# Kernel tuning notes

Hardware: AMD Instinct MI355X
Metric: run time of the kernel (lower is better)

The kernel has to match this reference:

```python
import jax, jax.numpy as jnp
import numpy as np


def _scan_dir(x, Wk, Wr, b):
    # x: (B,H,W,C) already flipped for the direction; Wk:(C,4U) Wr:(U,4U) b:(4U,)
    B, H, W, C = x.shape
    U = Wr.shape[0]
    Dmax = min(H, W)          # max anti-diagonal length
    D = H + W - 1             # number of anti-diagonals
    dt = x.dtype
    k = jnp.arange(Dmax)

    def step(carry, d):
        h1, c1, h2, c2 = carry            # diag d-1 and d-2 buffers, (B,Dmax,U)
        i0 = jnp.maximum(0, d - (W - 1))  # first row on diag d
        i1 = jnp.minimum(H - 1, d)        # last row on diag d
        rows = i0 + k
        cols = d - rows
        mask = rows <= i1                 # valid lanes on this diagonal
        rs = jnp.clip(rows, 0, H - 1)
        cs = jnp.clip(cols, 0, W - 1)
        x_diag = x[:, rs, cs, :]          # (B,Dmax,C)
        i0p = jnp.maximum(0, d - W)       # i0 of diag d-1
        i0pp = jnp.maximum(0, d - 1 - W)  # i0 of diag d-2

        def nb(buf, r_nb, lane0, extra):
            v = mask & extra
            lane = jnp.clip(r_nb - lane0, 0, Dmax - 1)
            g = jnp.take(buf, lane, axis=1)
            return jnp.where(v[None, :, None], g, jnp.zeros_like(g)), v

        up_ok = rows - 1 >= 0
        left_ok = cols - 1 >= 0
        h_up, v_up = nb(h1, rows - 1, i0p, up_ok)        # (i-1, j)   on diag d-1
        h_left, v_left = nb(h1, rows, i0p, left_ok)      # (i, j-1)   on diag d-1
        h_ul, v_ul = nb(h2, rows - 1, i0pp, up_ok & left_ok)  # (i-1,j-1) diag d-2
        c_up, _ = nb(c1, rows - 1, i0p, up_ok)
        c_left, _ = nb(c1, rows, i0p, left_ok)
        c_ul, _ = nb(c2, rows - 1, i0pp, up_ok & left_ok)

        cnt = (v_up.astype(dt) + v_left.astype(dt) + v_ul.astype(dt))[None, :, None]
        cnt = jnp.maximum(cnt, jnp.asarray(1.0, dt))
        h_prev = (h_up + h_left + h_ul) / cnt
        c_prev = (c_up + c_left + c_ul) / cnt

        # keras LSTMCell math, gate order i,f,g,o
        z = x_diag @ Wk + h_prev @ Wr + b
        zi, zf, zg, zo = jnp.split(z, 4, axis=-1)
        c_new = jax.nn.sigmoid(zf) * c_prev + jax.nn.sigmoid(zi) * jnp.tanh(zg)
        h_new = jax.nn.sigmoid(zo) * jnp.tanh(c_new)
        m = mask[None, :, None]
        h_new = jnp.where(m, h_new, jnp.zeros_like(h_new))
        c_new = jnp.where(m, c_new, jnp.zeros_like(c_new))
        return (h_new, c_new, h1, c1), h_new

    z0 = jnp.zeros((B, Dmax, U), dt)
    _, hs = jax.lax.scan(step, (z0, z0, z0, z0), jnp.arange(D))  # (D,B,Dmax,U)

    # scatter diagonal buffers back into the (B,H,W,U) grid (static indices)
    d_arr = np.arange(D)[:, None]
    kk = np.arange(Dmax)[None, :]
    rows_all = np.maximum(0, d_arr - (W - 1)) + kk
    cols_all = d_arr - rows_all
    valid = rows_all <= np.minimum(H - 1, d_arr)
    rws = np.where(valid, rows_all, H)   # invalid lanes -> padding row H
    cws = np.where(valid, cols_all, 0)
    out = jnp.zeros((B, H + 1, W, U), dt)
    out = out.at[:, rws, cws].set(jnp.transpose(hs, (1, 0, 2, 3)))
    return out[:, :H]


_FLIPS = [(False, False), (False, True), (True, False), (True, True)]  # SE,SW,NE,NW


def _forward(x, Wk, Wr, b):
    outs = []
    for i, (fh, fw) in enumerate(_FLIPS):
        xx = x
        if fh:
            xx = xx[:, ::-1]
        if fw:
            xx = xx[:, :, ::-1]
        o = _scan_dir(xx, Wk[i], Wr[i], b[i])
        if fw:
            o = o[:, :, ::-1]
        if fh:
            o = o[:, ::-1]
        outs.append(o)
    return jnp.concatenate(outs, axis=-1)


def setup_inputs() -> dict:
    key = jax.random.key(0)
    k0, k1, k2, k3 = jax.random.split(key, 4)
    B, H, W, C, U = 4, 128, 128, 64, 64
    x = jax.random.normal(k0, (B, H, W, C), jnp.float32)
    Wk = jax.random.normal(k1, (4, C, 4 * U), jnp.float32) * 0.08
    Wr = jax.random.normal(k2, (4, U, 4 * U), jnp.float32) * 0.08
    b = jax.random.normal(k3, (4, 4 * U), jnp.float32) * 0.02
    return {"x": x, "Wk": Wk, "Wr": Wr, "b": b}


def reference(x, Wk, Wr, b):
    return _forward(x, Wk, Wr, b)
```

## Files before the change

### kernel.cpp

```cpp
#include <hip/hip_runtime.h>

typedef __bf16 bf16x8 __attribute__((ext_vector_type(8)));
typedef __bf16 bf16x4 __attribute__((ext_vector_type(4)));
typedef float f32x4 __attribute__((ext_vector_type(4)));
typedef unsigned long long u64;

#define NCH 8
#define CELLS 16
#define NG 256
#define L2E 1.44269504089f
#define RDEPTH 16
#define NLINK (16 * 7)
#define RING_U64 (NLINK * RDEPTH * 64)
#define PROG_OFF (RING_U64 * 8)

__device__ __forceinline__ unsigned short f2bfbits(float f) {
  __bf16 b = (__bf16)f;
  return __builtin_bit_cast(unsigned short, b);
}
__device__ __forceinline__ float bfbits2f(unsigned short s) {
  return (float)__builtin_bit_cast(__bf16, s);
}
__device__ __forceinline__ void barrier_lds() {
  asm volatile("s_waitcnt lgkmcnt(0)" ::: "memory");
  __builtin_amdgcn_s_barrier();
}
__device__ __forceinline__ int hix(int row, int byteoff) {
  return row * 128 + (byteoff ^ ((row & 7) << 4));
}

__global__ __launch_bounds__(512, 1) void mdrnn_kernel(
    const float* __restrict__ x, const float* __restrict__ Wk,
    const float* __restrict__ Wr, const float* __restrict__ bias,
    float* __restrict__ out, char* __restrict__ ws) {
  __shared__ __align__(16) unsigned char xt[3][CELLS * 128];
  __shared__ __align__(16) unsigned char Pbuf[2][CELLS * 128];
  __shared__ __align__(16) unsigned char gbh[8 * 128];
  __shared__ __align__(16) float gbc[8 * 64];
  __shared__ __align__(16) float zbuf[2][4096];
  __shared__ __align__(16) u64 pubbuf[2][64];

  u64* __restrict__ ring = (u64*)ws;
  int* __restrict__ prog = (int*)(ws + PROG_OFF);

  const int tid = threadIdx.x;
  const bool isComp = (tid < 256);
  const int L = tid & 63;
  const int lo16 = L & 15;
  const int hi16 = L >> 4;
  const int wq = (tid >> 6) & 3;
  const int u = wq * 16 + lo16;
  const int hm0 = (tid >> 4) & 15;
  const int hq16 = tid & 15;

  const int ch = blockIdx.x >> 4;
  const int g = blockIdx.x & 15;
  const int f = g >> 2;
  const int bb = g & 3;
  const int fh = (f >> 1) & 1;
  const int fw = f & 1;
  const int R0 = ch * CELLS;
  const int D1 = R0 + 142;
  const int linkDn = g * 7 + ch - 1;
  const int linkUp = g * 7 + ch;

  for (int i = tid; i < 3 * CELLS * 32; i += 512) ((int*)xt)[i] = 0;
  for (int i = tid; i < 2 * CELLS * 32; i += 512) ((int*)Pbuf)[i] = 0;
  for (int i = tid; i < 8 * 32; i += 512) ((int*)gbh)[i] = 0;
  for (int i = tid; i < 8 * 64; i += 512) gbc[i] = 0.f;

  float bsc[4] = {0.f, 0.f, 0.f, 0.f};
  bf16x8 wkh[4][2], wrh[4][2], wrl[4][2];
  int oidx[4];
  int oStep = 0, cbase = 0;
  int o_ph0 = 0, o_ph1 = 0;
  int o_pw[4] = {0, 0, 0, 0};
  if (isComp) {
    const float* Wrf = Wr + f * (64 * NG);
#pragma unroll
    for (int t = 0; t < 4; ++t) {
      const float st = (t == 2) ? (2.f * L2E) : L2E;
#pragma unroll
      for (int kt = 0; kt < 2; ++kt)
#pragma unroll
        for (int jj = 0; jj < 8; ++jj) {
          int k = kt * 32 + hi16 * 8 + jj;
          float vr = Wrf[k * NG + t * 64 + u] * st;
          __bf16 vh = (__bf16)vr;
          wrh[t][kt][jj] = vh;
          wrl[t][kt][jj] = (__bf16)(vr - (float)vh);
        }
    }
    const int ccStep = fw ? -1 : 1;
#pragma unroll
    for (int j = 0; j < 4; ++j) {
      int ro = R0 + hi16 * 4 + j;
      int rr = fh ? 127 - ro : ro;
      int c0 = R0 - ro;
      oidx[j] = ((bb * 128 + rr) * 128 + (fw ? 127 - c0 : c0)) * NG + f * 64 + u;
      o_pw[j] = hix(hi16 * 4 + j, u * 2);
    }
    oStep = ccStep * NG;
    cbase = -hi16 * 4;
    o_ph0 = hix(lo16, hi16 * 16);
    o_ph1 = hix(lo16, 64 + hi16 * 16);
  } else {
    const float* Wkf = Wk + f * (64 * NG);
#pragma unroll
    for (int t = 0; t < 4; ++t) {
      const float st = (t == 2) ? (2.f * L2E) : L2E;
      bsc[t] = bias[f * NG + t * 64 + u] * st;
#pragma unroll
      for (int kt = 0; kt < 2; ++kt)
#pragma unroll
        for (int jj = 0; jj < 8; ++jj) {
          int k = kt * 32 + hi16 * 8 + jj;
          wkh[t][kt][jj] = (__bf16)(Wkf[k * NG + t * 64 + u] * st);
        }
    }
  }
  const int o_ax0 = hix(lo16, hi16 * 16);
  const int o_ax1 = hix(lo16, 64 + hi16 * 16);

  const int ccStepH = fw ? -1 : 1;
  const int rx = R0 + hm0;
  const int rrx = fh ? 127 - rx : rx;
  int cx = R0 - rx;
  int xidx = ((bb * 128 + rrx) * 128 + (fw ? 127 - cx : cx)) * 64 + hq16 * 4;
  const int xStep = ccStepH * 64;
  float4 px;
  bool pxv = false;
  auto ldg = [&]() {
    pxv = ((unsigned)cx <= 127u);
    px = make_float4(0.f, 0.f, 0.f, 0.f);
    if (pxv) px = *(const float4*)(x + xidx);
    xidx += xStep;
    ++cx;
  };
  auto stx = [&](unsigned char* buf) {
    if (pxv) {
      bf16x4 pk;
      pk[0] = (__bf16)px.x; pk[1] = (__bf16)px.y;
      pk[2] = (__bf16)px.z; pk[3] = (__bf16)px.w;
      *(bf16x4*)(buf + hix(hm0, hq16 * 8)) = pk;
    }
  };
  auto accx = [&](const unsigned char* xp, int bi) {
    bf16x8 a0 = *(const bf16x8*)(xp + o_ax0);
    bf16x8 a1 = *(const bf16x8*)(xp + o_ax1);
    float* zw = &zbuf[bi][0] + (wq * 64 + L) * 4;
#pragma unroll
    for (int t = 0; t < 4; ++t) {
      f32x4 az = (f32x4){bsc[t], bsc[t], bsc[t], bsc[t]};
      az = __builtin_amdgcn_mfma_f32_16x16x32_bf16(a0, wkh[t][0], az, 0, 0, 0);
      az = __builtin_amdgcn_mfma_f32_16x16x32_bf16(a1, wkh[t][1], az, 0, 0, 0);
      *(f32x4*)(zw + t * 1024) = az;
    }
  };

  __syncthreads();

  if (!isComp) {
    ldg();
    stx(&xt[R0 % 3][0]);
    ldg();
  }
  __syncthreads();

  if (!isComp) {
    stx(&xt[(R0 + 1) % 3][0]);
    ldg();
    accx(&xt[R0 % 3][0], R0 & 1);
    if (wq == 0 && ch > 0) {
#pragma unroll
      for (int k = 0; k < 4; ++k) {
        const int q = R0 - 1 + k;
        u64* src = ring + ((linkDn * RDEPTH + (q & (RDEPTH - 1))) << 6) + L;
        u64 v;
        int spin = 0;
        for (;;) {
          v = __hip_atomic_load(src, __ATOMIC_RELAXED, __HIP_MEMORY_SCOPE_AGENT);
          if ((unsigned short)(v >> 48) == (unsigned short)q ||
              spin >= (1 << 22))
            break;
          ++spin;
          __builtin_amdgcn_s_sleep(2);
        }
        *(unsigned short*)(gbh + (q & 7) * 128 + L * 2) =
            (unsigned short)(v >> 32);
        gbc[(q & 7) * 64 + L] = __uint_as_float((unsigned)v);
        if (k == 0)
          *(unsigned short*)(&Pbuf[(R0 + 1) & 1][0] + L * 2) =
              (unsigned short)(v >> 32);
      }
      if (L == 0)
        __hip_atomic_store(&prog[linkDn * 16], R0 + 2, __ATOMIC_RELAXED,
                           __HIP_MEMORY_SCOPE_AGENT);
    }
  }
  __syncthreads();

  f32x4 zacc[4];
  float hnprev[4];
  float csj[4];
  float puv[4];
  int gateSeen = 0;
  if (isComp) {
    const float* zb = &zbuf[R0 & 1][0] + (wq * 64 + L) * 4;
#pragma unroll
    for (int t = 0; t < 4; ++t) zacc[t] = *(const f32x4*)(zb + t * 1024);
    const float cu0 = gbc[((R0 - 1) & 7) * 64 + u];
#pragma unroll
    for (int j = 0; j < 4; ++j) {
      const float ci = (hi16 == 0 && j == 0) ? cu0 : 0.f;
      csj[j] = ci;
      puv[j] = ci;
      hnprev[j] = 0.f;
    }
    __builtin_amdgcn_s_setprio(1);
  } else {
    accx(&xt[(R0 + 1) % 3][0], (R0 + 1) & 1);
    stx(&xt[(R0 + 2) % 3][0]);
    ldg();
  }
  __syncthreads();

  unsigned char* Pc = &Pbuf[R0 & 1][0];
  unsigned char* Pp = &Pbuf[(R0 + 1) & 1][0];
  unsigned char* xA = &xt[(R0 + 2) % 3][0];
  unsigned char* xB = &xt[R0 % 3][0];
  unsigned char* xC = &xt[(R0 + 1) % 3][0];

  for (int d = R0; d <= D1; ++d) {
    if (isComp) {
      bf16x8 pa0 = *(const bf16x8*)(Pp + o_ph0);
      bf16x8 pa1 = *(const bf16x8*)(Pp + o_ph1);
      const float gh1 = bfbits2f(*(const unsigned short*)(gbh + (d & 7) * 128 + u * 2));
      const float gh2 = bfbits2f(*(const unsigned short*)(gbh + ((d - 1) & 7) * 128 + u * 2));
      const float gc1 = gbc[(d & 7) * 64 + u];
#pragma unroll
      for (int t = 0; t < 4; ++t)
        zacc[t] = __builtin_amdgcn_mfma_f32_16x16x32_bf16(pa0, wrh[t][0], zacc[t], 0, 0, 0);
#pragma unroll
      for (int t = 0; t < 4; ++t)
        zacc[t] = __builtin_amdgcn_mfma_f32_16x16x32_bf16(pa1, wrh[t][1], zacc[t], 0, 0, 0);
#pragma unroll
      for (int t = 0; t < 4; ++t)
        zacc[t] = __builtin_amdgcn_mfma_f32_16x16x32_bf16(pa0, wrl[t][0], zacc[t], 0, 0, 0);
#pragma unroll
      for (int t = 0; t < 4; ++t)
        zacc[t] = __builtin_amdgcn_mfma_f32_16x16x32_bf16(pa1, wrl[t][1], zacc[t], 0, 0, 0);

      const bool pubW = (ch < NCH - 1) && (d >= R0 + 15);

      float hcur[4], cnew[4];
      {
        const int lm = hi16 * 4 + 3;
        const int cj = cbase - 3;
        const bool ok = ((unsigned)cj <= 127u);
        const float inv = (cj == 0 || (R0 + lm) == 0) ? 1.f : (1.f / 3.f);
        const float cpj = csj[3] * inv;
        const float e1 = __builtin_amdgcn_exp2f(-zacc[1][3]);
        const float e2 = __builtin_amdgcn_exp2f(-zacc[0][3]);
        const float e3 = __builtin_amdgcn_exp2f(zacc[2][3]);
        float cn = cpj * __builtin_amdgcn_rcpf(1.f + e1) +
                   (e3 - 1.f) * __builtin_amdgcn_rcpf((1.f + e2) * (1.f + e3));
        const float e4 = __builtin_amdgcn_exp2f(-zacc[3][3]);
        const float e5 = __builtin_amdgcn_exp2f(2.f * L2E * cn);
        float hn = (e5 - 1.f) * __builtin_amdgcn_rcpf((1.f + e4) * (1.f + e5));
        if (pubW && lm == CELLS - 1)
          pubbuf[d & 1][u] = ((u64)(unsigned short)d << 48) |
                             ((u64)f2bfbits(hn) << 32) |
                             (u64)__float_as_uint(cn);
        hn = ok ? hn : 0.f;
        cn = ok ? cn : 0.f;
        hcur[3] = hn;
        cnew[3] = cn;
        if (ok) out[oidx[3]] = hn;
      }
      const unsigned pk =
          ((unsigned)f2bfbits(hcur[3]) << 16) | f2bfbits(hnprev[3]);
      const unsigned pku = __shfl((int)pk, (L - 16) & 63);
      const float up_c = __shfl(cnew[3], (L - 16) & 63);
#pragma unroll
      for (int jj = 0; jj < 3; ++jj) {
        const int j = 2 - jj;
        const int lm = hi16 * 4 + j;
        const int cj = cbase - j;
        const bool ok = ((unsigned)cj <= 127u);
        const float inv = (cj == 0 || (R0 + lm) == 0) ? 1.f : (1.f / 3.f);
        const float cpj = csj[j] * inv;
        const float e1 = __builtin_amdgcn_exp2f(-zacc[1][j]);
        const float e2 = __builtin_amdgcn_exp2f(-zacc[0][j]);
        const float e3 = __builtin_amdgcn_exp2f(zacc[2][j]);
        float cn = cpj * __builtin_amdgcn_rcpf(1.f + e1) +
                   (e3 - 1.f) * __builtin_amdgcn_rcpf((1.f + e2) * (1.f + e3));
        const float e4 = __builtin_amdgcn_exp2f(-zacc[3][j]);
        const float e5 = __builtin_amdgcn_exp2f(2.f * L2E * cn);
        float hn = (e5 - 1.f) * __builtin_amdgcn_rcpf((1.f + e4) * (1.f + e5));
        hn = ok ? hn : 0.f;
        cn = ok ? cn : 0.f;
        hcur[j] = hn;
        cnew[j] = cn;
        if (ok) out[oidx[j]] = hn;
      }
      const float up_h = bfbits2f((unsigned short)(pku >> 16));
      const float up_hp = bfbits2f((unsigned short)(pku & 0xffff));

#pragma unroll
      for (int j = 0; j < 4; ++j) {
        const float hup = j ? hcur[j - 1] : (hi16 ? up_h : gh1);
        const float hulp = j ? hnprev[j - 1] : (hi16 ? up_hp : gh2);
        const float sPj =
            ((cbase + 1 == j) || (R0 == 0 && hi16 == 0 && j == 0))
                ? 1.f : (1.f / 3.f);
        *(unsigned short*)(Pc + o_pw[j]) =
            f2bfbits(sPj * (hup + hcur[j] + hulp));
        const float cun = j ? cnew[j - 1] : (hi16 ? up_c : gc1);
        csj[j] = cun + cnew[j] + puv[j];
        puv[j] = cun;
      }
#pragma unroll
      for (int j = 0; j < 4; ++j) {
        hnprev[j] = hcur[j];
        oidx[j] += oStep;
      }
      ++cbase;

      const float* zb = &zbuf[(d + 1) & 1][0] + (wq * 64 + L) * 4;
#pragma unroll
      for (int t = 0; t < 4; ++t) zacc[t] = *(const f32x4*)(zb + t * 1024);
    } else {
      const bool meAct = (ch > 0) && (wq == ((d - R0) & 1));
      const int q = d + 3;
      const bool qLive = meAct && (q <= R0 + 126);
      const u64* qs = ring + ((linkDn * RDEPTH + (q & (RDEPTH - 1))) << 6) + L;
      u64 qv = 0;
      if (qLive)
        qv = __hip_atomic_load(qs, __ATOMIC_RELAXED, __HIP_MEMORY_SCOPE_AGENT);

      if (wq == 0 && ch < NCH - 1) {
        const int pd = d - 1;
        if (pd >= R0 + 15) {
          if (pd >= R0 + 15 + RDEPTH && gateSeen < pd - RDEPTH) {
            int spin = 0;
            do {
              gateSeen = __hip_atomic_load(&prog[linkUp * 16], __ATOMIC_RELAXED,
                                           __HIP_MEMORY_SCOPE_AGENT);
              if (gateSeen < pd - RDEPTH) __builtin_amdgcn_s_sleep(1);
            } while (gateSeen < pd - RDEPTH && ++spin < (1 << 22));
          }
          u64 v = pubbuf[(d - 1) & 1][L];
          u64* dst = ring + ((linkUp * RDEPTH + (pd & (RDEPTH - 1))) << 6) + L;
          __hip_atomic_store(dst, v, __ATOMIC_RELAXED,
                             __HIP_MEMORY_SCOPE_AGENT);
        }
      }
      accx(xA, (d + 2) & 1);
      stx(xB);
      ldg();
      if (qLive) {
        int spin = 0;
        while ((unsigned short)(qv >> 48) != (unsigned short)q &&
               spin < (1 << 22)) {
          ++spin;
          __builtin_amdgcn_s_sleep(1);
          qv = __hip_atomic_load(qs, __ATOMIC_RELAXED,
                                 __HIP_MEMORY_SCOPE_AGENT);
        }
        *(unsigned short*)(gbh + (q & 7) * 128 + L * 2) =
            (unsigned short)(qv >> 32);
        gbc[(q & 7) * 64 + L] = __uint_as_float((unsigned)qv);
      }
      if (meAct && L == 0)
        __hip_atomic_store(&prog[linkDn * 16], min(d + 3, R0 + 126),
                           __ATOMIC_RELAXED, __HIP_MEMORY_SCOPE_AGENT);
    }

    {
      unsigned char* t0 = xA; xA = xB; xB = xC; xC = t0;
      unsigned char* t1 = Pc; Pc = Pp; Pp = t1;
    }
    barrier_lds();
  }

  if (!isComp && wq == 0 && ch < NCH - 1) {
    const int pd = D1;
    if (pd >= R0 + 15 + RDEPTH && gateSeen < pd - RDEPTH) {
      int spin = 0;
      do {
        gateSeen = __hip_atomic_load(&prog[linkUp * 16], __ATOMIC_RELAXED,
                                     __HIP_MEMORY_SCOPE_AGENT);
        if (gateSeen < pd - RDEPTH) __builtin_amdgcn_s_sleep(1);
      } while (gateSeen < pd - RDEPTH && ++spin < (1 << 22));
    }
    u64 v = pubbuf[D1 & 1][L];
    u64* dst = ring + ((linkUp * RDEPTH + (pd & (RDEPTH - 1))) << 6) + L;
    __hip_atomic_store(dst, v, __ATOMIC_RELAXED, __HIP_MEMORY_SCOPE_AGENT);
  }
}

extern "C" void kernel_launch(void* const* d_in, const int* in_sizes, int n_in,
                              void* d_out, int out_size, void* d_ws, size_t ws_size,
                              hipStream_t stream) {
  const float* x = (const float*)d_in[0];
  const float* Wk = (const float*)d_in[1];
  const float* Wr = (const float*)d_in[2];
  const float* b = (const float*)d_in[3];
  float* out = (float*)d_out;
  hipMemsetAsync(d_ws, 0, PROG_OFF + NLINK * 16 * sizeof(int), stream);
  hipLaunchKernelGGL(mdrnn_kernel, dim3(128), dim3(512), 0, stream, x, Wk, Wr,
                     b, out, (char*)d_ws);
}
```

Measured before the change: 260.7 us.

## Publish boundary state directly from compute warps and prefetch ring gate check

Compute lanes now write their boundary h/c values straight into the inter-block ring buffer at the same step, instead of staging them in LDS for a helper warp to forward one diagonal later. The ring-slot gate check moves to a different helper warp and is performed ahead of time for the next diagonal, with its atomic load issued early so the spin overlaps other work. The cell math also merges two reciprocals into one, and output stores are moved after the neighbour update. This cuts one diagonal of latency from the cross-block pipeline, at the cost of more fragile ordering between the gate wait and the direct publish.

Result: faster. 234.9 us (-9.9%).

```diff
diff --git a/kernel.cpp b/kernel.cpp
--- a/kernel.cpp
+++ b/kernel.cpp
@@ -38,7 +38,6 @@
   __shared__ __align__(16) unsigned char gbh[8 * 128];
   __shared__ __align__(16) float gbc[8 * 64];
   __shared__ __align__(16) float zbuf[2][4096];
-  __shared__ __align__(16) u64 pubbuf[2][64];
 
   u64* __restrict__ ring = (u64*)ws;
   int* __restrict__ prog = (int*)(ws + PROG_OFF);
@@ -255,28 +254,29 @@
 
       float hcur[4], cnew[4];
       {
-        const int lm = hi16 * 4 + 3;
         const int cj = cbase - 3;
         const bool ok = ((unsigned)cj <= 127u);
-        const float inv = (cj == 0 || (R0 + lm) == 0) ? 1.f : (1.f / 3.f);
+        const float inv = (cj == 0) ? 1.f : (1.f / 3.f);
         const float cpj = csj[3] * inv;
         const float e1 = __builtin_amdgcn_exp2f(-zacc[1][3]);
         const float e2 = __builtin_amdgcn_exp2f(-zacc[0][3]);
         const float e3 = __builtin_amdgcn_exp2f(zacc[2][3]);
-        float cn = cpj * __builtin_amdgcn_rcpf(1.f + e1) +
-                   (e3 - 1.f) * __builtin_amdgcn_rcpf((1.f + e2) * (1.f + e3));
+        const float A = 1.f + e1, Bv = 1.f + e2, Cv = 1.f + e3;
+        const float BC = Bv * Cv;
+        float cn = (cpj * BC + (e3 - 1.f) * A) *
+                   __builtin_amdgcn_rcpf(A * BC);
         const float e4 = __builtin_amdgcn_exp2f(-zacc[3][3]);
         const float e5 = __builtin_amdgcn_exp2f(2.f * L2E * cn);
         float hn = (e5 - 1.f) * __builtin_amdgcn_rcpf((1.f + e4) * (1.f + e5));
-        if (pubW && lm == CELLS - 1)
-          pubbuf[d & 1][u] = ((u64)(unsigned short)d << 48) |
-                             ((u64)f2bfbits(hn) << 32) |
-                             (u64)__float_as_uint(cn);
-        hn = ok ? hn : 0.f;
-        cn = ok ? cn : 0.f;
-        hcur[3] = hn;
-        cnew[3] = cn;
-        if (ok) out[oidx[3]] = hn;
+        if (pubW && hi16 == 3) {
+          u64 v = ((u64)(unsigned short)d << 48) | ((u64)f2bfbits(hn) << 32) |
+                  (u64)__float_as_uint(cn);
+          u64* dst = ring + ((linkUp * RDEPTH + (d & (RDEPTH - 1))) << 6) + u;
+          __hip_atomic_store(dst, v, __ATOMIC_RELAXED,
+                             __HIP_MEMORY_SCOPE_AGENT);
+        }
+        hcur[3] = ok ? hn : 0.f;
+        cnew[3] = ok ? cn : 0.f;
       }
       const unsigned pk =
           ((unsigned)f2bfbits(hcur[3]) << 16) | f2bfbits(hnprev[3]);
@@ -285,24 +285,23 @@
 #pragma unroll
       for (int jj = 0; jj < 3; ++jj) {
         const int j = 2 - jj;
-        const int lm = hi16 * 4 + j;
         const int cj = cbase - j;
         const bool ok = ((unsigned)cj <= 127u);
-        const float inv = (cj == 0 || (R0 + lm) == 0) ? 1.f : (1.f / 3.f);
+        const float inv =
+            (cj == 0 || (j == 0 && R0 == 0 && hi16 == 0)) ? 1.f : (1.f / 3.f);
         const float cpj = csj[j] * inv;
         const float e1 = __builtin_amdgcn_exp2f(-zacc[1][j]);
         const float e2 = __builtin_amdgcn_exp2f(-zacc[0][j]);
         const float e3 = __builtin_amdgcn_exp2f(zacc[2][j]);
-        float cn = cpj * __builtin_amdgcn_rcpf(1.f + e1) +
-                   (e3 - 1.f) * __builtin_amdgcn_rcpf((1.f + e2) * (1.f + e3));
+        const float A = 1.f + e1, Bv = 1.f + e2, Cv = 1.f + e3;
+        const float BC = Bv * Cv;
+        float cn = (cpj * BC + (e3 - 1.f) * A) *
+                   __builtin_amdgcn_rcpf(A * BC);
         const float e4 = __builtin_amdgcn_exp2f(-zacc[3][j]);
         const float e5 = __builtin_amdgcn_exp2f(2.f * L2E * cn);
         float hn = (e5 - 1.f) * __builtin_amdgcn_rcpf((1.f + e4) * (1.f + e5));
-        hn = ok ? hn : 0.f;
-        cn = ok ? cn : 0.f;
-        hcur[j] = hn;
-        cnew[j] = cn;
-        if (ok) out[oidx[j]] = hn;
+        hcur[j] = ok ? hn : 0.f;
+        cnew[j] = ok ? cn : 0.f;
       }
       const float up_h = bfbits2f((unsigned short)(pku >> 16));
       const float up_hp = bfbits2f((unsigned short)(pku & 0xffff));
@@ -322,6 +321,7 @@
       }
 #pragma unroll
       for (int j = 0; j < 4; ++j) {
+        if ((unsigned)(cbase - j) <= 127u) out[oidx[j]] = hcur[j];
         hnprev[j] = hcur[j];
         oidx[j] += oStep;
       }
@@ -338,27 +338,18 @@
       u64 qv = 0;
       if (qLive)
         qv = __hip_atomic_load(qs, __ATOMIC_RELAXED, __HIP_MEMORY_SCOPE_AGENT);
-
-      if (wq == 0 && ch < NCH - 1) {
-        const int pd = d - 1;
-        if (pd >= R0 + 15) {
-          if (pd >= R0 + 15 + RDEPTH && gateSeen < pd - RDEPTH) {
-            int spin = 0;
-            do {
-              gateSeen = __hip_atomic_load(&prog[linkUp * 16], __ATOMIC_RELAXED,
-                                           __HIP_MEMORY_SCOPE_AGENT);
-              if (gateSeen < pd - RDEPTH) __builtin_amdgcn_s_sleep(1);
-            } while (gateSeen < pd - RDEPTH && ++spin < (1 << 22));
-          }
-          u64 v = pubbuf[(d - 1) & 1][L];
-          u64* dst = ring + ((linkUp * RDEPTH + (pd & (RDEPTH - 1))) << 6) + L;
-          __hip_atomic_store(dst, v, __ATOMIC_RELAXED,
-                             __HIP_MEMORY_SCOPE_AGENT);
-        }
-      }
+      const int nt = d + 1;
+      const bool gatev = (wq == 2) && (ch < NCH - 1) && (nt <= D1) &&
+                         (nt >= R0 + 15 + RDEPTH);
+      int progNow = gateSeen;
+      if (gatev && gateSeen < nt - RDEPTH)
+        progNow = __hip_atomic_load(&prog[linkUp * 16], __ATOMIC_RELAXED,
+                                    __HIP_MEMORY_SCOPE_AGENT);
+
       accx(xA, (d + 2) & 1);
       stx(xB);
       ldg();
+
       if (qLive) {
         int spin = 0;
         while ((unsigned short)(qv >> 48) != (unsigned short)q &&
@@ -375,6 +366,16 @@
       if (meAct && L == 0)
         __hip_atomic_store(&prog[linkDn * 16], min(d + 3, R0 + 126),
                            __ATOMIC_RELAXED, __HIP_MEMORY_SCOPE_AGENT);
+      if (gatev) {
+        if (progNow > gateSeen) gateSeen = progNow;
+        int spin = 0;
+        while (gateSeen < nt - RDEPTH && spin < (1 << 22)) {
+          ++spin;
+          __builtin_amdgcn_s_sleep(1);
+          gateSeen = __hip_atomic_load(&prog[linkUp * 16], __ATOMIC_RELAXED,
+                                       __HIP_MEMORY_SCOPE_AGENT);
+        }
+      }
     }
 
     {
@@ -382,21 +383,6 @@
       unsigned char* t1 = Pc; Pc = Pp; Pp = t1;
     }
     barrier_lds();
-  }
-
-  if (!isComp && wq == 0 && ch < NCH - 1) {
-    const int pd = D1;
-    if (pd >= R0 + 15 + RDEPTH && gateSeen < pd - RDEPTH) {
-      int spin = 0;
-      do {
-        gateSeen = __hip_atomic_load(&prog[linkUp * 16], __ATOMIC_RELAXED,
-                                     __HIP_MEMORY_SCOPE_AGENT);
-        if (gateSeen < pd - RDEPTH) __builtin_amdgcn_s_sleep(1);
-      } while (gateSeen < pd - RDEPTH && ++spin < (1 << 22));
-    }
-    u64 v = pubbuf[D1 & 1][L];
-    u64* dst = ring + ((linkUp * RDEPTH + (pd & (RDEPTH - 1))) << 6) + L;
-    __hip_atomic_store(dst, v, __ATOMIC_RELAXED, __HIP_MEMORY_SCOPE_AGENT);
   }
 }
 
```
